# Kernel tuning notes

Hardware: AMD Instinct MI355X
Metric: run time of the kernel (lower is better)

Reference implementation:

```python
import jax, jax.numpy as jnp
import numpy as np


def dct_matrix(n):
    # orthonormal DCT-II matrix, matches scipy.fftpack.dct(norm='ortho')
    k = jnp.arange(n, dtype=jnp.float32)[:, None]
    i = jnp.arange(n, dtype=jnp.float32)[None, :]
    D = jnp.cos(jnp.pi * (2.0 * i + 1.0) * k / (2.0 * n))
    s = jnp.where(k == 0, jnp.sqrt(1.0 / n), jnp.sqrt(2.0 / n))
    return (D * s).astype(jnp.float32)


def mad_mask(h, w):
    eps = 1e-10
    v1 = int(min(h, w) * 0.1)
    v2 = int(min(h, w) * 0.7)
    v3 = min(h, w)
    xy = jnp.maximum(jnp.arange(h, dtype=jnp.float32)[:, None],
                     jnp.arange(w, dtype=jnp.float32)[None, :])
    m = jnp.where(xy <= v1, 1.0 - xy / (v1 + eps) * 0.95,
        jnp.where(xy <= v2, 0.01,
        jnp.where(xy <= v3, (xy - v2) / (v3 - v2) * 0.3, 0.5)))
    return m.astype(jnp.float32)


def setup_inputs() -> dict:
    key = jax.random.key(0)
    ks = jax.random.split(key, 8)
    num_layers, token_length, C = 24, 100, 1024
    N, B = 1024, 32  # h = w = 32
    patch = 16
    val = np.sqrt(6.0 / float(3 * patch * patch + C))
    feats = jax.random.normal(ks[0], (1 + N, B, C), dtype=jnp.float32)
    learnable_tokens = jax.random.uniform(ks[1], (num_layers, token_length, C),
                                          minval=-val, maxval=val, dtype=jnp.float32)
    lim = 1.0 / np.sqrt(C)
    W_t2f = jax.random.uniform(ks[2], (C, C), minval=-lim, maxval=lim, dtype=jnp.float32)
    b_t2f = jax.random.uniform(ks[3], (C,), minval=-lim, maxval=lim, dtype=jnp.float32)
    W_df = jax.random.uniform(ks[4], (C, C), minval=-lim, maxval=lim, dtype=jnp.float32)
    b_df = jax.random.uniform(ks[5], (C,), minval=-lim, maxval=lim, dtype=jnp.float32)
    return {
        'feats': feats,
        'layer': 5,
        'learnable_tokens': learnable_tokens,
        'scale': jnp.float32(0.001),
        'W_t2f': W_t2f,
        'b_t2f': b_t2f,
        'W_df': W_df,
        'b_df': b_df,
    }


def reference(feats, layer, learnable_tokens, scale, W_t2f, b_t2f, W_df, b_df):
    # has_cls_token=True, batch_first=False (defaults)
    cls_tok, x = feats[:1], feats[1:]          # [1,B,C], [N,B,C]
    N, B, C = x.shape
    h = int(np.sqrt(N)); w = h
    # NOTE: original does a raw reshape (N,B,C) -> (B,C,h,w); replicate faithfully.
    ximg = x.reshape(B, C, h, w)
    # --- MAD_decompose: 2D orthonormal DCT-II per (b, c) image ---
    D = dct_matrix(h)
    feat_dct = jnp.einsum('ik,bckl,jl->bcij', D, ximg, D)
    mask = mad_mask(h, w)                      # [h,w]
    cal = feat_dct * (1.0 - mask)              # high-frequency (causal) part
    cal = cal.reshape(N, B, C)                 # raw reshape as in torch code
    # --- forward_delta_feat ---
    tokens = learnable_tokens[layer]           # [M,C]
    attn = jnp.einsum('nbc,mc->nbm', cal, tokens) * (C ** -0.5)
    attn = jax.nn.softmax(attn, axis=-1)
    t2f = tokens[1:] @ W_t2f.T + b_t2f         # [M-1,C]
    df = jnp.einsum('nbm,mc->nbc', attn[:, :, 1:], t2f)
    df = (df + cal) @ W_df.T + b_df            # [N,B,C]
    # --- MAD_compose_fast: ifft2 approximation of IDCT, clamp to [0,255] ---
    fc = df.reshape(B, C, h, w).astype(jnp.complex64)
    out = jnp.clip(jnp.real(jnp.fft.ifft2(fc, norm='ortho')), 0.0, 255.0)
    out = out.reshape(N, B, C).astype(jnp.float32)
    x = x + out * scale
    return jnp.concatenate([cls_tok, x], axis=0)
```

## Files before the change

kernel.cpp:

```cpp
#include <hip/hip_runtime.h>

typedef unsigned short u16;
typedef u16 ushort8 __attribute__((ext_vector_type(8)));
typedef u16 ushort4v __attribute__((ext_vector_type(4)));
typedef __bf16 bf16x8 __attribute__((ext_vector_type(8)));
typedef float f32x4 __attribute__((ext_vector_type(4)));

#define PI_F 3.14159265358979323846f

__device__ __forceinline__ u16 f2bf(float f) {
  union { float f; unsigned int u; } v; v.f = f;
  unsigned int r = v.u + 0x7fffu + ((v.u >> 16) & 1u);
  return (u16)(r >> 16);
}
__device__ __forceinline__ float bf2f(u16 u) {
  union { unsigned int u; float f; } v; v.u = ((unsigned int)u) << 16;
  return v.f;
}

__device__ __forceinline__ void gload16(const u16* g, u16* l) {
  __builtin_amdgcn_global_load_lds((const __attribute__((address_space(1))) void*)g,
                                   (__attribute__((address_space(3))) void*)l, 16, 0, 0);
}

__device__ __forceinline__ void stage_tile(const u16* __restrict__ G, int ld, int row0, int k0,
                                           u16* lds, int wid, int lane) {
  int seg = wid * 32;
  const u16* gp = G + (size_t)(row0 + seg + (lane >> 2)) * ld + k0 + (lane & 3) * 8;
  gload16(gp, lds + seg * 32);
  gload16(gp + (size_t)16 * ld, lds + (seg + 16) * 32);
}

__device__ __forceinline__ float im_val(int r, int c) {
  float xy = (float)(r > c ? r : c);
  float m = (xy <= 3.0f) ? (1.0f - xy * (0.95f / 3.0f))
           : ((xy <= 22.0f) ? 0.01f : ((xy - 22.0f) * 0.03f));
  return 1.0f - m;
}
__device__ __forceinline__ float dct_val(int r, int c) {
  int a = ((2 * c + 1) * r) & 127;
  float s = (r == 0) ? 0.17677669529663687f : 0.25f;
  return cosf((float)a * (PI_F / 64.0f)) * s;
}

__global__ __launch_bounds__(256) void k_prep(const float* __restrict__ feats,
                                              const float* __restrict__ lt, const int* __restrict__ layerp,
                                              const float* __restrict__ Wt2f,
                                              u16* __restrict__ xb, u16* __restrict__ wt_bf,
                                              u16* __restrict__ tok_bf, u16* __restrict__ A2,
                                              float* __restrict__ outp) {
  int tid = blockIdx.x * 256 + threadIdx.x;
  int L = *layerp;
  const float4* in4 = (const float4*)(feats + 32768);
  ushort4v* xb4 = (ushort4v*)xb;
  #pragma unroll
  for (int rep = 0; rep < 16; ++rep) {
    int j = tid + rep * 524288;
    float4 v = in4[j];
    ushort4v o;
    o[0] = f2bf(v.x); o[1] = f2bf(v.y); o[2] = f2bf(v.z); o[3] = f2bf(v.w);
    xb4[j] = o;
  }
  ((ushort8*)A2)[tid] = (ushort8){0,0,0,0,0,0,0,0};
  if (tid < 262144) {
    float4 v = ((const float4*)Wt2f)[tid];
    ushort4v o;
    o[0] = f2bf(v.x); o[1] = f2bf(v.y); o[2] = f2bf(v.z); o[3] = f2bf(v.w);
    ((ushort4v*)wt_bf)[tid] = o;
  }
  if (tid < 32768) {
    outp[tid] = feats[tid];
    int m = tid >> 8;
    ushort4v o = (ushort4v){0,0,0,0};
    if (m < 99) {
      float4 v = *(const float4*)(lt + (size_t)L * 102400 + (size_t)(m + 1) * 1024 + (tid & 255) * 4);
      o[0] = f2bf(v.x); o[1] = f2bf(v.y); o[2] = f2bf(v.z); o[3] = f2bf(v.w);
    }
    ((ushort4v*)tok_bf)[tid] = o;
  }
}

__device__ void mdct_row(const float* __restrict__ row, u16* __restrict__ dst, float* sm, int t) {
  float* Ms = sm; float* T1 = sm + 1056; float* Dsh = sm + 2112;
  for (int i = t; i < 1024; i += 256) {
    int r = i >> 5, c = i & 31;
    Dsh[r * 33 + c] = dct_val(r, c);
    Ms[r * 33 + c] = row[i] * im_val(r, c);
  }
  __syncthreads();
  int k = t >> 3, l0 = (t & 7) * 4;
  float a0 = 0, a1 = 0, a2 = 0, a3 = 0;
  #pragma unroll 8
  for (int i = 0; i < 32; ++i) {
    float d = Dsh[i * 33 + k];
    const float* mr = &Ms[i * 33 + l0];
    a0 += d * mr[0]; a1 += d * mr[1]; a2 += d * mr[2]; a3 += d * mr[3];
  }
  T1[k * 33 + l0 + 0] = a0; T1[k * 33 + l0 + 1] = a1;
  T1[k * 33 + l0 + 2] = a2; T1[k * 33 + l0 + 3] = a3;
  __syncthreads();
  float b0 = 0, b1 = 0, b2 = 0, b3 = 0;
  #pragma unroll 8
  for (int j = 0; j < 32; ++j) {
    float u = T1[k * 33 + j];
    b0 += u * Dsh[j * 33 + l0 + 0];
    b1 += u * Dsh[j * 33 + l0 + 1];
    b2 += u * Dsh[j * 33 + l0 + 2];
    b3 += u * Dsh[j * 33 + l0 + 3];
  }
  ushort4v o;
  o[0] = f2bf(b0); o[1] = f2bf(b1); o[2] = f2bf(b2); o[3] = f2bf(b3);
  *(ushort4v*)(dst + k * 32 + l0) = o;
}

__global__ __launch_bounds__(256) void k_setupA(const float* __restrict__ Wdf, const float* __restrict__ bdf,
                                                const float* __restrict__ lt, const int* __restrict__ layerp,
                                                float* __restrict__ weff_f, u16* __restrict__ weff_bf,
                                                float* __restrict__ beff, u16* __restrict__ tok2) {
  __shared__ __align__(16) float sm[14784];
  int bid = blockIdx.x, t = threadIdx.x;
  if (bid < 256) {
    float* In = sm; float* Uc = sm + 4224; float* Us = sm + 8448;
    float* Csh = sm + 12672; float* Ssh = sm + 13728;
    int c0 = bid * 4;
    for (int i = t; i < 1024; i += 256) {
      int r = i >> 5, c = i & 31;
      float ang = (float)((r * c) & 31) * (PI_F / 16.0f);
      Csh[r * 33 + c] = cosf(ang); Ssh[r * 33 + c] = sinf(ang);
    }
    { int cc = t & 3, v0 = t >> 2;
      for (int v = v0; v < 1024; v += 64)
        In[cc * 1056 + (v >> 5) * 33 + (v & 31)] = Wdf[(size_t)v * 1024 + c0 + cc]; }
    __syncthreads();
    int cc = t >> 6, L2 = t & 63, p = L2 & 31, h = L2 >> 5;
    for (int j = h * 16; j < h * 16 + 16; ++j) {
      float ac = 0, as = 0;
      #pragma unroll 8
      for (int i = 0; i < 32; ++i) {
        float m = In[cc * 1056 + i * 33 + j];
        ac += Csh[p * 33 + i] * m;
        as += Ssh[p * 33 + i] * m;
      }
      Uc[cc * 1056 + p * 33 + j] = ac;
      Us[cc * 1056 + p * 33 + j] = as;
    }
    __syncthreads();
    for (int q = h * 16; q < h * 16 + 16; ++q) {
      float acc = 0;
      #pragma unroll 8
      for (int j = 0; j < 32; ++j)
        acc += Uc[cc * 1056 + p * 33 + j] * Csh[q * 33 + j] -
               Us[cc * 1056 + p * 33 + j] * Ssh[q * 33 + j];
      float val = acc * 0.03125f;
      size_t idx = (size_t)(p * 32 + q) * 1024 + c0 + cc;
      weff_f[idx] = val;
      weff_bf[idx] = f2bf(val);
    }
  } else if (bid == 256) {
    float* Bsh = sm; float* Uc = sm + 1056; float* Us = sm + 2112;
    float* Csh = sm + 3168; float* Ssh = sm + 4224;
    for (int i = t; i < 1024; i += 256) {
      int r = i >> 5, c = i & 31;
      float ang = (float)((r * c) & 31) * (PI_F / 16.0f);
      Csh[r * 33 + c] = cosf(ang); Ssh[r * 33 + c] = sinf(ang);
      Bsh[r * 33 + c] = bdf[i];
    }
    __syncthreads();
    for (int idx = t; idx < 1024; idx += 256) {
      int p = idx >> 5, j = idx & 31;
      float ac = 0, as = 0;
      #pragma unroll 8
      for (int i = 0; i < 32; ++i) {
        float m = Bsh[i * 33 + j];
        ac += Csh[p * 33 + i] * m;
        as += Ssh[p * 33 + i] * m;
      }
      Uc[p * 33 + j] = ac; Us[p * 33 + j] = as;
    }
    __syncthreads();
    for (int idx = t; idx < 1024; idx += 256) {
      int p = idx >> 5, q = idx & 31;
      float acc = 0;
      #pragma unroll 8
      for (int jj = 0; jj < 32; ++jj)
        acc += Uc[p * 33 + jj] * Csh[q * 33 + jj] - Us[p * 33 + jj] * Ssh[q * 33 + jj];
      beff[idx] = acc * 0.03125f;
    }
  } else {
    int p = bid - 257;
    if (p >= 100) {
      *(ushort4v*)(tok2 + (size_t)p * 1024 + t * 4) = (ushort4v){0,0,0,0};
      return;
    }
    mdct_row(lt + (size_t)(*layerp) * 102400 + (size_t)p * 1024, tok2 + (size_t)p * 1024, sm, t);
  }
}

template <int NT>
__device__ __forceinline__ void gemm128_core(const u16* __restrict__ A, int lda,
                                             const u16* __restrict__ B, int ldb,
                                             int g0, int c0, u16* sA, u16* sB,
                                             f32x4 (&acc)[4][4], int wid, int lane) {
  int wr = wid >> 1, wc = wid & 1, cl = lane & 15, rg = lane >> 4;
  stage_tile(A, lda, g0, 0, sA, wid, lane);
  stage_tile(B, ldb, c0, 0, sB, wid, lane);
  __syncthreads();
  #pragma unroll 1
  for (int kt = 0; kt < NT; ++kt) {
    int cur = kt & 1;
    if (kt + 1 < NT) {
      stage_tile(A, lda, g0, (kt + 1) * 32, sA + (cur ^ 1) * 4096, wid, lane);
      stage_tile(B, ldb, c0, (kt + 1) * 32, sB + (cur ^ 1) * 4096, wid, lane);
    }
    const u16* pa = sA + cur * 4096;
    const u16* pb = sB + cur * 4096;
    bf16x8 af[4], bv[4];
    #pragma unroll
    for (int mf = 0; mf < 4; mf++)
      af[mf] = *(const bf16x8*)(pa + (wr * 64 + mf * 16 + cl) * 32 + rg * 8);
    #pragma unroll
    for (int nf = 0; nf < 4; nf++)
      bv[nf] = *(const bf16x8*)(pb + (wc * 64 + nf * 16 + cl) * 32 + rg * 8);
    #pragma unroll
    for (int mf = 0; mf < 4; mf++)
      #pragma unroll
      for (int nf = 0; nf < 4; nf++)
        acc[mf][nf] = __builtin_amdgcn_mfma_f32_16x16x32_bf16(af[mf], bv[nf], acc[mf][nf], 0, 0, 0);
    __syncthreads();
  }
}

__global__ __launch_bounds__(256) void k_setupB(const float* __restrict__ weff_f,
                                                const u16* __restrict__ tok_bf, const u16* __restrict__ wt_bf,
                                                const float* __restrict__ bt2f,
                                                u16* __restrict__ w2, u16* __restrict__ t2f) {
  __shared__ __align__(16) u16 smem[16384];
  int bid = blockIdx.x, t = threadIdx.x;
  if (bid < 1024) {
    mdct_row(weff_f + (size_t)bid * 1024, w2 + (size_t)bid * 1024, (float*)smem, t);
  } else {
    int bn = bid - 1024;
    int lane = t & 63, wid = t >> 6;
    int wr = wid >> 1, wc = wid & 1, cl = lane & 15, rg = lane >> 4;
    f32x4 acc[4][4];
    #pragma unroll
    for (int i = 0; i < 4; i++)
      #pragma unroll
      for (int j = 0; j < 4; j++) acc[i][j] = (f32x4){0.f,0.f,0.f,0.f};
    gemm128_core<32>(tok_bf, 1024, wt_bf, 1024, 0, bn * 128, smem, smem + 8192, acc, wid, lane);
    #pragma unroll
    for (int mf = 0; mf < 4; mf++)
      #pragma unroll
      for (int nf = 0; nf < 4; nf++) {
        int col = bn * 128 + wc * 64 + nf * 16 + cl;
        #pragma unroll
        for (int r = 0; r < 4; r++) {
          int row = wr * 64 + mf * 16 + rg * 4 + r;
          t2f[(size_t)row * 1024 + col] = (row < 99) ? f2bf(acc[mf][nf][r] + bt2f[col]) : (u16)0;
        }
      }
  }
}

__global__ __launch_bounds__(256) void k_setupC(const u16* __restrict__ weff_bf, const u16* __restrict__ t2f,
                                                const u16* __restrict__ xb, const u16* __restrict__ tok2,
                                                u16* __restrict__ Gt, u16* __restrict__ A2) {
  __shared__ __align__(16) u16 smem[16384];
  int bid = blockIdx.x, t = threadIdx.x;
  int lane = t & 63, wid = t >> 6;
  if (bid < 8) {
    int wr = wid >> 1, wc = wid & 1, cl = lane & 15, rg = lane >> 4;
    f32x4 acc[4][4];
    #pragma unroll
    for (int i = 0; i < 4; i++)
      #pragma unroll
      for (int j = 0; j < 4; j++) acc[i][j] = (f32x4){0.f,0.f,0.f,0.f};
    gemm128_core<32>(weff_bf, 1024, t2f, 1024, bid * 128, 0, smem, smem + 8192, acc, wid, lane);
    #pragma unroll
    for (int mf = 0; mf < 4; mf++)
      #pragma unroll
      for (int nf = 0; nf < 4; nf++) {
        int col = wc * 64 + nf * 16 + cl;
        #pragma unroll
        for (int r = 0; r < 4; r++) {
          int row = bid * 128 + wr * 64 + mf * 16 + rg * 4 + r;
          Gt[(size_t)row * 128 + col] = f2bf(acc[mf][nf][r]);
        }
      }
  } else {
    int g0 = (bid - 8) * 128;
    int cl = lane & 15, rg = lane >> 4;
    u16* sA = smem; u16* sB = smem + 8192;
    f32x4 acc[2][7];
    #pragma unroll
    for (int i = 0; i < 2; i++)
      #pragma unroll
      for (int j = 0; j < 7; j++) acc[i][j] = (f32x4){0.f,0.f,0.f,0.f};
    stage_tile(xb, 1024, g0, 0, sA, wid, lane);
    stage_tile(tok2, 1024, 0, 0, sB, wid, lane);
    __syncthreads();
    #pragma unroll 1
    for (int kt = 0; kt < 32; ++kt) {
      int cur = kt & 1;
      if (kt + 1 < 32) {
        stage_tile(xb, 1024, g0, (kt + 1) * 32, sA + (cur ^ 1) * 4096, wid, lane);
        stage_tile(tok2, 1024, 0, (kt + 1) * 32, sB + (cur ^ 1) * 4096, wid, lane);
      }
      const u16* pa = sA + cur * 4096;
      const u16* pb = sB + cur * 4096;
      bf16x8 a0 = *(const bf16x8*)(pa + (wid * 32 + cl) * 32 + rg * 8);
      bf16x8 a1 = *(const bf16x8*)(pa + (wid * 32 + 16 + cl) * 32 + rg * 8);
      #pragma unroll
      for (int nf = 0; nf < 7; nf++) {
        bf16x8 bv = *(const bf16x8*)(pb + (nf * 16 + cl) * 32 + rg * 8);
        acc[0][nf] = __builtin_amdgcn_mfma_f32_16x16x32_bf16(a0, bv, acc[0][nf], 0, 0, 0);
        acc[1][nf] = __builtin_amdgcn_mfma_f32_16x16x32_bf16(a1, bv, acc[1][nf], 0, 0, 0);
      }
      __syncthreads();
    }
    #pragma unroll
    for (int mf = 0; mf < 2; mf++) {
      #pragma unroll
      for (int r = 0; r < 4; r++) {
        int grow = g0 + wid * 32 + mf * 16 + rg * 4 + r;
        float v[7];
        float mx = -1e30f;
        #pragma unroll
        for (int nf = 0; nf < 7; nf++) {
          int m = nf * 16 + cl;
          v[nf] = acc[mf][nf][r] * 0.03125f;
          if (m < 100) mx = fmaxf(mx, v[nf]);
        }
        #pragma unroll
        for (int d = 1; d < 16; d <<= 1) mx = fmaxf(mx, __shfl_xor(mx, d));
        float s = 0;
        #pragma unroll
        for (int nf = 0; nf < 7; nf++) {
          int m = nf * 16 + cl;
          float e = (m < 100) ? __expf(v[nf] - mx) : 0.0f;
          v[nf] = e; s += e;
        }
        #pragma unroll
        for (int d = 1; d < 16; d <<= 1) s += __shfl_xor(s, d);
        float inv = 1.0f / s;
        #pragma unroll
        for (int nf = 0; nf < 7; nf++) {
          int m = nf * 16 + cl;
          if (m >= 1 && m < 100) A2[(size_t)grow * 128 + (m - 1)] = f2bf(v[nf] * inv);
        }
      }
    }
  }
}

__global__ __launch_bounds__(256) void k_main(const u16* __restrict__ xb, const u16* __restrict__ w2,
                                              const u16* __restrict__ a2, const u16* __restrict__ gt,
                                              const float* __restrict__ beff, const float* __restrict__ feats,
                                              const float* __restrict__ scalep, float* __restrict__ outf) {
  __shared__ __align__(16) u16 smem[16384];
  u16* sA = smem; u16* sB = smem + 8192;
  int t = threadIdx.x, lane = t & 63, wid = t >> 6;
  int bid = blockIdx.x;
  int xcd = bid & 7, local = bid >> 3;
  int super = local >> 5, within = local & 31;
  int bm = xcd * 32 + super * 4 + (within & 3);
  int bn = within >> 2;
  int g0 = bm * 128, c0 = bn * 128;
  int wr = wid >> 1, wc = wid & 1;
  int cl = lane & 15, rg = lane >> 4;
  f32x4 acc[4][4];
  #pragma unroll
  for (int i = 0; i < 4; i++)
    #pragma unroll
    for (int j = 0; j < 4; j++) acc[i][j] = (f32x4){0.f,0.f,0.f,0.f};

  auto stage = [&](int kt, int b) {
    if (kt < 32) {
      stage_tile(xb, 1024, g0, kt * 32, sA + b * 4096, wid, lane);
      stage_tile(w2, 1024, c0, kt * 32, sB + b * 4096, wid, lane);
    } else {
      int k0 = (kt - 32) * 32;
      stage_tile(a2, 128, g0, k0, sA + b * 4096, wid, lane);
      stage_tile(gt, 128, c0, k0, sB + b * 4096, wid, lane);
    }
  };

  stage(0, 0);
  __syncthreads();
  #pragma unroll 1
  for (int kt = 0; kt < 36; ++kt) {
    int cur = kt & 1;
    if (kt + 1 < 36) stage(kt + 1, cur ^ 1);
    const u16* pa = sA + cur * 4096;
    const u16* pb = sB + cur * 4096;
    bf16x8 af[4], bv[4];
    #pragma unroll
    for (int mf = 0; mf < 4; mf++)
      af[mf] = *(const bf16x8*)(pa + (wr * 64 + mf * 16 + cl) * 32 + rg * 8);
    #pragma unroll
    for (int nf = 0; nf < 4; nf++)
      bv[nf] = *(const bf16x8*)(pb + (wc * 64 + nf * 16 + cl) * 32 + rg * 8);
    #pragma unroll
    for (int mf = 0; mf < 4; mf++)
      #pragma unroll
      for (int nf = 0; nf < 4; nf++)
        acc[mf][nf] = __builtin_amdgcn_mfma_f32_16x16x32_bf16(af[mf], bv[nf], acc[mf][nf], 0, 0, 0);
    __syncthreads();
  }

  float sc = *scalep;
  #pragma unroll
  for (int mf = 0; mf < 4; mf++) {
    #pragma unroll
    for (int nf = 0; nf < 4; nf++) {
      int col = c0 + wc * 64 + nf * 16 + cl;
      #pragma unroll
      for (int r = 0; r < 4; r++) {
        int row = g0 + wr * 64 + mf * 16 + rg * 4 + r;
        size_t idx = (size_t)row * 1024 + col;
        float val = acc[mf][nf][r] + beff[col];
        float rr = fminf(fmaxf(val, 0.f), 255.f);
        outf[32768 + idx] = feats[32768 + idx] + rr * sc;
      }
    }
  }
}

extern "C" void kernel_launch(void* const* d_in, const int* in_sizes, int n_in,
                              void* d_out, int out_size, void* d_ws, size_t ws_size,
                              hipStream_t stream) {
  const float* feats  = (const float*)d_in[0];
  const int*   layerp = (const int*)d_in[1];
  const float* lt     = (const float*)d_in[2];
  const float* scalep = (const float*)d_in[3];
  const float* Wt2f   = (const float*)d_in[4];
  const float* bt2f   = (const float*)d_in[5];
  const float* Wdf    = (const float*)d_in[6];
  const float* bdf    = (const float*)d_in[7];
  float* outp = (float*)d_out;

  char* ws = (char*)d_ws;
  float* beff   = (float*)(ws + 0);
  float* weff_f = (float*)(ws + 65536);
  u16* weff_bf = (u16*)(ws + 4259840);
  u16* w2      = (u16*)(ws + 6356992);
  u16* tok_bf  = (u16*)(ws + 8454144);
  u16* wt_bf   = (u16*)(ws + 8716288);
  u16* tok2    = (u16*)(ws + 10813440);
  u16* t2f     = (u16*)(ws + 11075584);
  u16* Gt      = (u16*)(ws + 11337728);
  u16* A2      = (u16*)(ws + 11599872);
  u16* xb      = (u16*)(ws + 19988480);

  k_prep<<<2048, 256, 0, stream>>>(feats, lt, layerp, Wt2f, xb, wt_bf, tok_bf, A2, outp);
  k_setupA<<<385, 256, 0, stream>>>(Wdf, bdf, lt, layerp, weff_f, weff_bf, beff, tok2);
  k_setupB<<<1032, 256, 0, stream>>>(weff_f, tok_bf, wt_bf, bt2f, w2, t2f);
  k_setupC<<<264, 256, 0, stream>>>(weff_bf, t2f, xb, tok2, Gt, A2);
  k_main<<<2048, 256, 0, stream>>>(xb, w2, A2, Gt, beff, feats, scalep, outp);
}
```

Baseline: 254.3 us.

## Triple-buffer LDS staging with vmcnt-based waits and a single barrier per k-step

Replaces the double-buffered global-to-LDS staging in all three GEMM paths with a three-slot ring. Each step prefetches two tiles ahead and waits with s_waitcnt vmcnt(4) and one raw s_barrier instead of two __syncthreads, so loads overlap more with MFMA work. This raises LDS use per block from 32KB to 48KB, which may lower occupancy. Correctness depends on the compiler not reordering or adding outstanding vector-memory operations beyond what the hand-written vmcnt counts assume.

```diff
diff --git a/kernel.cpp b/kernel.cpp
--- a/kernel.cpp
+++ b/kernel.cpp
@@ -30,6 +30,9 @@
   gload16(gp, lds + seg * 32);
   gload16(gp + (size_t)16 * ld, lds + (seg + 16) * 32);
 }
+
+#define WAIT_VM(N) asm volatile("s_waitcnt vmcnt(" #N ")" ::: "memory")
+#define RAW_BARRIER() asm volatile("s_barrier" ::: "memory")
 
 __device__ __forceinline__ float im_val(int r, int c) {
   float xy = (float)(r > c ? r : c);
@@ -199,21 +202,25 @@
 template <int NT>
 __device__ __forceinline__ void gemm128_core(const u16* __restrict__ A, int lda,
                                              const u16* __restrict__ B, int ldb,
-                                             int g0, int c0, u16* sA, u16* sB,
+                                             int g0, int c0, u16* smem,
                                              f32x4 (&acc)[4][4], int wid, int lane) {
   int wr = wid >> 1, wc = wid & 1, cl = lane & 15, rg = lane >> 4;
-  stage_tile(A, lda, g0, 0, sA, wid, lane);
-  stage_tile(B, ldb, c0, 0, sB, wid, lane);
-  __syncthreads();
+  stage_tile(A, lda, g0, 0, smem, wid, lane);
+  stage_tile(B, ldb, c0, 0, smem + 12288, wid, lane);
+  stage_tile(A, lda, g0, 32, smem + 4096, wid, lane);
+  stage_tile(B, ldb, c0, 32, smem + 16384, wid, lane);
+  int cur = 0;
   #pragma unroll 1
   for (int kt = 0; kt < NT; ++kt) {
-    int cur = kt & 1;
-    if (kt + 1 < NT) {
-      stage_tile(A, lda, g0, (kt + 1) * 32, sA + (cur ^ 1) * 4096, wid, lane);
-      stage_tile(B, ldb, c0, (kt + 1) * 32, sB + (cur ^ 1) * 4096, wid, lane);
-    }
-    const u16* pa = sA + cur * 4096;
-    const u16* pb = sB + cur * 4096;
+    if (kt == NT - 1) { WAIT_VM(0); } else { WAIT_VM(4); }
+    RAW_BARRIER();
+    if (kt + 2 < NT) {
+      int slot = (cur == 0) ? 2 : cur - 1;
+      stage_tile(A, lda, g0, (kt + 2) * 32, smem + slot * 4096, wid, lane);
+      stage_tile(B, ldb, c0, (kt + 2) * 32, smem + 12288 + slot * 4096, wid, lane);
+    }
+    const u16* pa = smem + cur * 4096;
+    const u16* pb = smem + 12288 + cur * 4096;
     bf16x8 af[4], bv[4];
     #pragma unroll
     for (int mf = 0; mf < 4; mf++)
@@ -226,7 +233,7 @@
       #pragma unroll
       for (int nf = 0; nf < 4; nf++)
         acc[mf][nf] = __builtin_amdgcn_mfma_f32_16x16x32_bf16(af[mf], bv[nf], acc[mf][nf], 0, 0, 0);
-    __syncthreads();
+    cur = (cur == 2) ? 0 : cur + 1;
   }
 }
 
@@ -234,7 +241,7 @@
                                                 const u16* __restrict__ tok_bf, const u16* __restrict__ wt_bf,
                                                 const float* __restrict__ bt2f,
                                                 u16* __restrict__ w2, u16* __restrict__ t2f) {
-  __shared__ __align__(16) u16 smem[16384];
+  __shared__ __align__(16) u16 smem[24576];
   int bid = blockIdx.x, t = threadIdx.x;
   if (bid < 1024) {
     mdct_row(weff_f + (size_t)bid * 1024, w2 + (size_t)bid * 1024, (float*)smem, t);
@@ -247,7 +254,7 @@
     for (int i = 0; i < 4; i++)
       #pragma unroll
       for (int j = 0; j < 4; j++) acc[i][j] = (f32x4){0.f,0.f,0.f,0.f};
-    gemm128_core<32>(tok_bf, 1024, wt_bf, 1024, 0, bn * 128, smem, smem + 8192, acc, wid, lane);
+    gemm128_core<32>(tok_bf, 1024, wt_bf, 1024, 0, bn * 128, smem, acc, wid, lane);
     #pragma unroll
     for (int mf = 0; mf < 4; mf++)
       #pragma unroll
@@ -265,7 +272,7 @@
 __global__ __launch_bounds__(256) void k_setupC(const u16* __restrict__ weff_bf, const u16* __restrict__ t2f,
                                                 const u16* __restrict__ xb, const u16* __restrict__ tok2,
                                                 u16* __restrict__ Gt, u16* __restrict__ A2) {
-  __shared__ __align__(16) u16 smem[16384];
+  __shared__ __align__(16) u16 smem[24576];
   int bid = blockIdx.x, t = threadIdx.x;
   int lane = t & 63, wid = t >> 6;
   if (bid < 8) {
@@ -275,7 +282,7 @@
     for (int i = 0; i < 4; i++)
       #pragma unroll
       for (int j = 0; j < 4; j++) acc[i][j] = (f32x4){0.f,0.f,0.f,0.f};
-    gemm128_core<32>(weff_bf, 1024, t2f, 1024, bid * 128, 0, smem, smem + 8192, acc, wid, lane);
+    gemm128_core<32>(weff_bf, 1024, t2f, 1024, bid * 128, 0, smem, acc, wid, lane);
     #pragma unroll
     for (int mf = 0; mf < 4; mf++)
       #pragma unroll
@@ -290,24 +297,27 @@
   } else {
     int g0 = (bid - 8) * 128;
     int cl = lane & 15, rg = lane >> 4;
-    u16* sA = smem; u16* sB = smem + 8192;
     f32x4 acc[2][7];
     #pragma unroll
     for (int i = 0; i < 2; i++)
       #pragma unroll
       for (int j = 0; j < 7; j++) acc[i][j] = (f32x4){0.f,0.f,0.f,0.f};
-    stage_tile(xb, 1024, g0, 0, sA, wid, lane);
-    stage_tile(tok2, 1024, 0, 0, sB, wid, lane);
-    __syncthreads();
+    stage_tile(xb, 1024, g0, 0, smem, wid, lane);
+    stage_tile(tok2, 1024, 0, 0, smem + 12288, wid, lane);
+    stage_tile(xb, 1024, g0, 32, smem + 4096, wid, lane);
+    stage_tile(tok2, 1024, 0, 32, smem + 16384, wid, lane);
+    int cur = 0;
     #pragma unroll 1
     for (int kt = 0; kt < 32; ++kt) {
-      int cur = kt & 1;
-      if (kt + 1 < 32) {
-        stage_tile(xb, 1024, g0, (kt + 1) * 32, sA + (cur ^ 1) * 4096, wid, lane);
-        stage_tile(tok2, 1024, 0, (kt + 1) * 32, sB + (cur ^ 1) * 4096, wid, lane);
-      }
-      const u16* pa = sA + cur * 4096;
-      const u16* pb = sB + cur * 4096;
+      if (kt == 31) { WAIT_VM(0); } else { WAIT_VM(4); }
+      RAW_BARRIER();
+      if (kt + 2 < 32) {
+        int slot = (cur == 0) ? 2 : cur - 1;
+        stage_tile(xb, 1024, g0, (kt + 2) * 32, smem + slot * 4096, wid, lane);
+        stage_tile(tok2, 1024, 0, (kt + 2) * 32, smem + 12288 + slot * 4096, wid, lane);
+      }
+      const u16* pa = smem + cur * 4096;
+      const u16* pb = smem + 12288 + cur * 4096;
       bf16x8 a0 = *(const bf16x8*)(pa + (wid * 32 + cl) * 32 + rg * 8);
       bf16x8 a1 = *(const bf16x8*)(pa + (wid * 32 + 16 + cl) * 32 + rg * 8);
       #pragma unroll
@@ -316,7 +326,7 @@
         acc[0][nf] = __builtin_amdgcn_mfma_f32_16x16x32_bf16(a0, bv, acc[0][nf], 0, 0, 0);
         acc[1][nf] = __builtin_amdgcn_mfma_f32_16x16x32_bf16(a1, bv, acc[1][nf], 0, 0, 0);
       }
-      __syncthreads();
+      cur = (cur == 2) ? 0 : cur + 1;
     }
     #pragma unroll
     for (int mf = 0; mf < 2; mf++) {
@@ -357,8 +367,7 @@
                                               const u16* __restrict__ a2, const u16* __restrict__ gt,
                                               const float* __restrict__ beff, const float* __restrict__ feats,
                                               const float* __restrict__ scalep, float* __restrict__ outf) {
-  __shared__ __align__(16) u16 smem[16384];
-  u16* sA = smem; u16* sB = smem + 8192;
+  __shared__ __align__(16) u16 smem[24576];
   int t = threadIdx.x, lane = t & 63, wid = t >> 6;
   int bid = blockIdx.x;
   int xcd = bid & 7, local = bid >> 3;
@@ -374,25 +383,29 @@
     #pragma unroll
     for (int j = 0; j < 4; j++) acc[i][j] = (f32x4){0.f,0.f,0.f,0.f};
 
-  auto stage = [&](int kt, int b) {
+  auto stage = [&](int kt, int slot) {
+    u16* sa = smem + slot * 4096;
+    u16* sb = smem + 12288 + slot * 4096;
     if (kt < 32) {
-      stage_tile(xb, 1024, g0, kt * 32, sA + b * 4096, wid, lane);
-      stage_tile(w2, 1024, c0, kt * 32, sB + b * 4096, wid, lane);
+      stage_tile(xb, 1024, g0, kt * 32, sa, wid, lane);
+      stage_tile(w2, 1024, c0, kt * 32, sb, wid, lane);
     } else {
       int k0 = (kt - 32) * 32;
-      stage_tile(a2, 128, g0, k0, sA + b * 4096, wid, lane);
-      stage_tile(gt, 128, c0, k0, sB + b * 4096, wid, lane);
+      stage_tile(a2, 128, g0, k0, sa, wid, lane);
+      stage_tile(gt, 128, c0, k0, sb, wid, lane);
     }
   };
 
   stage(0, 0);
-  __syncthreads();
+  stage(1, 1);
+  int cur = 0;
   #pragma unroll 1
   for (int kt = 0; kt < 36; ++kt) {
-    int cur = kt & 1;
-    if (kt + 1 < 36) stage(kt + 1, cur ^ 1);
-    const u16* pa = sA + cur * 4096;
-    const u16* pb = sB + cur * 4096;
+    if (kt == 35) { WAIT_VM(0); } else { WAIT_VM(4); }
+    RAW_BARRIER();
+    if (kt + 2 < 36) stage(kt + 2, (cur == 0) ? 2 : cur - 1);
+    const u16* pa = smem + cur * 4096;
+    const u16* pb = smem + 12288 + cur * 4096;
     bf16x8 af[4], bv[4];
     #pragma unroll
     for (int mf = 0; mf < 4; mf++)
@@ -405,7 +418,7 @@
       #pragma unroll
       for (int nf = 0; nf < 4; nf++)
         acc[mf][nf] = __builtin_amdgcn_mfma_f32_16x16x32_bf16(af[mf], bv[nf], acc[mf][nf], 0, 0, 0);
-    __syncthreads();
+    cur = (cur == 2) ? 0 : cur + 1;
   }
 
   float sc = *scalep;
```

Result: faster. 246.8 us (-2.9%).
